# Performance work log

Measured on AMD Instinct MI355X. Metric: run time of the kernel, lower is better.

The kernel has to match this reference:

```python
import jax, jax.numpy as jnp
import numpy as np

N_HEADS = 8


def setup_inputs() -> dict:
    key = jax.random.key(0)
    qkv = jax.random.normal(key, (4, 1536, 2048), dtype=jnp.float32)
    return {"qkv": qkv}


def reference(qkv):
    bs, width, length = qkv.shape
    assert width % (3 * N_HEADS) == 0
    ch = width // (3 * N_HEADS)
    q, k, v = jnp.split(qkv, 3, axis=1)            # each [bs, H*C, T]
    scale = 1.0 / (ch ** 0.25)                      # 1/sqrt(sqrt(ch)) applied to both q and k
    q = (q * scale).reshape(bs * N_HEADS, ch, length)
    k = (k * scale).reshape(bs * N_HEADS, ch, length)
    v = v.reshape(bs * N_HEADS, ch, length)
    weight = jnp.einsum('bct,bcs->bts', q, k)       # [bs*H, T, T]
    weight = jax.nn.softmax(weight.astype(jnp.float32), axis=-1).astype(weight.dtype)
    a = jnp.einsum('bts,bcs->bct', weight, v)       # [bs*H, C, T]
    return a.reshape(bs, -1, length)
```

## Files before the change

kernel.cpp:

```cpp
#include <hip/hip_runtime.h>


typedef _Float16 half8  __attribute__((ext_vector_type(8)));
typedef _Float16 half4  __attribute__((ext_vector_type(4)));
typedef float    floatx4 __attribute__((ext_vector_type(4)));

constexpr int T    = 2048;
constexpr int TQ   = 128;
constexpr int TS   = 64;
constexpr int LDK  = 72;
constexpr int LDV  = 72;
constexpr int KHALF  = TS * LDK;
constexpr int SMEM_H = KHALF + 64 * LDV;
constexpr int NIT  = T / TS;
constexpr float QSCALE = 0.125f * 1.44269504088896340736f;

__device__ __forceinline__ half4 pack4(float a, float b, float c, float d) {
    half4 r;
    r[0] = (_Float16)a; r[1] = (_Float16)b;
    r[2] = (_Float16)c; r[3] = (_Float16)d;
    return r;
}

__global__ __launch_bounds__(512, 4)
void qkv_attn_kernel(const float* __restrict__ qkv, float* __restrict__ out) {
    __shared__ __align__(16) _Float16 smem[2][SMEM_H];

    const int tid  = threadIdx.x;
    const int wave = tid >> 6;
    const int lane = tid & 63;
    const int n16  = lane & 15;
    const int g    = lane >> 4;
    const int h    = wave >> 2;
    const int qg   = wave & 3;

    const int bx = blockIdx.x;
    const int hd = bx & 31;
    const int qt = bx >> 5;
    const int b  = hd >> 3;
    const int hh = hd & 7;
    const int q0 = qt * TQ;

    const float* __restrict__ qbase = qkv + (size_t)(b * 1536 + hh * 64) * T;
    const float* __restrict__ kbase = qkv + (size_t)(b * 1536 + 512 + hh * 64) * T;
    const float* __restrict__ vbase = qkv + (size_t)(b * 1536 + 1024 + hh * 64) * T;
    float* __restrict__ obase = out + (size_t)(b * 512 + hh * 64) * T;

    const bool kstage = (wave < 4);
    const int ptid = tid & 255;
    const int ks   = ((ptid >> 6) << 4) | (ptid & 15);
    const int kc4  = ((ptid >> 4) & 3) << 2;
    const int vc   = ptid >> 4;
    const int vt   = ptid & 15;
    const int vcol = 32 * (vt >> 3) + 8 * (vt & 3) + 4 * ((vt >> 2) & 1);

    float pre[16];
    auto prefetch = [&](int s0) {
        if (kstage) {
            const float* kg = kbase + s0 + ks;
#pragma unroll
            for (int i = 0; i < 4; ++i) {
                const int c = i * 16 + kc4;
#pragma unroll
                for (int j = 0; j < 4; ++j) pre[i * 4 + j] = kg[(c + j) * T];
            }
        } else {
            const float* vg = vbase + vc * T + s0 + vt * 4;
#pragma unroll
            for (int i = 0; i < 4; ++i) {
                const floatx4 vv = *(const floatx4*)&vg[i * 16 * T];
                pre[i * 4 + 0] = vv.x; pre[i * 4 + 1] = vv.y;
                pre[i * 4 + 2] = vv.z; pre[i * 4 + 3] = vv.w;
            }
        }
    };
    auto flush = [&](int buf) {
        if (kstage) {
            _Float16* kd = &smem[buf][ks * LDK];
#pragma unroll
            for (int i = 0; i < 4; ++i)
                *(half4*)&kd[i * 16 + kc4] =
                    pack4(pre[i * 4], pre[i * 4 + 1], pre[i * 4 + 2], pre[i * 4 + 3]);
        } else {
            _Float16* vd = &smem[buf][KHALF + vc * LDV + vcol];
#pragma unroll
            for (int i = 0; i < 4; ++i)
                *(half4*)&vd[i * 16 * LDV] =
                    pack4(pre[i * 4], pre[i * 4 + 1], pre[i * 4 + 2], pre[i * 4 + 3]);
        }
    };

    half8 bq[2][2];
    floatx4 oacc[4][2];
    float lsum[2];

#pragma unroll
    for (int qt2 = 0; qt2 < 2; ++qt2) {
        const int q = q0 + qg * 32 + qt2 * 16 + n16;
#pragma unroll
        for (int kcA = 0; kcA < 2; ++kcA)
#pragma unroll
            for (int j = 0; j < 8; ++j) {
                const int c = kcA * 32 + g * 8 + j;
                bq[qt2][kcA][j] = (_Float16)(qbase[c * T + q] * QSCALE);
            }
    }
#pragma unroll
    for (int mt = 0; mt < 4; ++mt)
#pragma unroll
        for (int qt2 = 0; qt2 < 2; ++qt2) oacc[mt][qt2] = (floatx4)(0.f);
    lsum[0] = 0.f; lsum[1] = 0.f;

    prefetch(0);
    flush(0);
    __syncthreads();

    for (int it = 0; it < NIT; ++it) {
        const int buf = it & 1;
        if (it + 1 < NIT) prefetch((it + 1) * TS);

        const _Float16* kb = &smem[buf][0];
        const _Float16* vb = &smem[buf][KHALF];

        floatx4 sacc[2][2];
#pragma unroll
        for (int sub = 0; sub < 2; ++sub) {
            const half8 ak0 = *(const half8*)&kb[((h * 2 + sub) * 16 + n16) * LDK + g * 8];
            const half8 ak1 = *(const half8*)&kb[((h * 2 + sub) * 16 + n16) * LDK + 32 + g * 8];
#pragma unroll
            for (int qt2 = 0; qt2 < 2; ++qt2) {
                floatx4 acc = (floatx4)(0.f);
                acc = __builtin_amdgcn_mfma_f32_16x16x32_f16(ak0, bq[qt2][0], acc, 0, 0, 0);
                acc = __builtin_amdgcn_mfma_f32_16x16x32_f16(ak1, bq[qt2][1], acc, 0, 0, 0);
                sacc[qt2][sub] = acc;
            }
        }
        half8 av[4];
#pragma unroll
        for (int mt = 0; mt < 4; ++mt)
            av[mt] = *(const half8*)&vb[(mt * 16 + n16) * LDV + h * 32 + g * 8];
#pragma unroll
        for (int qt2 = 0; qt2 < 2; ++qt2) {
            float pv[8];
#pragma unroll
            for (int sub = 0; sub < 2; ++sub)
#pragma unroll
                for (int r = 0; r < 4; ++r)
                    pv[sub * 4 + r] = __builtin_amdgcn_exp2f(sacc[qt2][sub][r]);
            lsum[qt2] += ((pv[0] + pv[1]) + (pv[2] + pv[3]))
                       + ((pv[4] + pv[5]) + (pv[6] + pv[7]));
            half8 bp;
#pragma unroll
            for (int i = 0; i < 8; ++i) bp[i] = (_Float16)pv[i];
#pragma unroll
            for (int mt = 0; mt < 4; ++mt)
                oacc[mt][qt2] = __builtin_amdgcn_mfma_f32_16x16x32_f16(
                    av[mt], bp, oacc[mt][qt2], 0, 0, 0);
        }

        if (it + 1 < NIT) flush(buf ^ 1);
        __syncthreads();
    }

    float* red = (float*)&smem[0][0];
    const int rbase = (qg * 64 + lane) * 36;
    if (h == 1) {
#pragma unroll
        for (int qt2 = 0; qt2 < 2; ++qt2)
#pragma unroll
            for (int mt = 0; mt < 4; ++mt)
                *(floatx4*)&red[rbase + (qt2 * 4 + mt) * 4] = oacc[mt][qt2];
        red[rbase + 32] = lsum[0];
        red[rbase + 33] = lsum[1];
    }
    __syncthreads();
    if (h == 0) {
#pragma unroll
        for (int qt2 = 0; qt2 < 2; ++qt2)
#pragma unroll
            for (int mt = 0; mt < 4; ++mt)
                oacc[mt][qt2] += *(const floatx4*)&red[rbase + (qt2 * 4 + mt) * 4];
        lsum[0] += red[rbase + 32];
        lsum[1] += red[rbase + 33];
#pragma unroll
        for (int qt2 = 0; qt2 < 2; ++qt2) {
            float l = lsum[qt2];
            l += __shfl_xor(l, 16);
            l += __shfl_xor(l, 32);
            const float linv = 1.0f / l;
            const int tcol = q0 + qg * 32 + qt2 * 16 + n16;
#pragma unroll
            for (int mt = 0; mt < 4; ++mt)
#pragma unroll
                for (int r = 0; r < 4; ++r)
                    obase[(mt * 16 + g * 4 + r) * T + tcol] = oacc[mt][qt2][r] * linv;
        }
    }
}

extern "C" void kernel_launch(void* const* d_in, const int* in_sizes, int n_in,
                              void* d_out, int out_size, void* d_ws, size_t ws_size,
                              hipStream_t stream) {
    const float* qkv = (const float*)d_in[0];
    float* out = (float*)d_out;
    qkv_attn_kernel<<<dim3(512), dim3(512), 0, stream>>>(qkv, out);
}
```

Measured before the change: 125.8 us.

## Halve query tile per block, double grid, and raise MFMA wave priority

The query tile per block drops from 128 to 64 rows, so each wave handles one 16-query sub-tile instead of two and the grid doubles to 1024 blocks. The launch-bounds occupancy hint rises from 4 to 8 blocks to match the lower register use. s_setprio is placed around the MFMA groups so matrix work is favoured over the loads of other waves. The trade-off is that each K/V tile is now fetched and converted to fp16 twice as often per query, which doubles global load and staging traffic for K and V.

```diff
diff --git a/kernel.cpp b/kernel.cpp
--- a/kernel.cpp
+++ b/kernel.cpp
@@ -6,7 +6,7 @@
 typedef float    floatx4 __attribute__((ext_vector_type(4)));
 
 constexpr int T    = 2048;
-constexpr int TQ   = 128;
+constexpr int TQ   = 64;
 constexpr int TS   = 64;
 constexpr int LDK  = 72;
 constexpr int LDV  = 72;
@@ -22,7 +22,7 @@
     return r;
 }
 
-__global__ __launch_bounds__(512, 4)
+__global__ __launch_bounds__(512, 8)
 void qkv_attn_kernel(const float* __restrict__ qkv, float* __restrict__ out) {
     __shared__ __align__(16) _Float16 smem[2][SMEM_H];
 
@@ -90,26 +90,22 @@
         }
     };
 
-    half8 bq[2][2];
-    floatx4 oacc[4][2];
-    float lsum[2];
+    half8 bq[2];
+    floatx4 oacc[4];
+    float lsum = 0.f;
 
-#pragma unroll
-    for (int qt2 = 0; qt2 < 2; ++qt2) {
-        const int q = q0 + qg * 32 + qt2 * 16 + n16;
+    {
+        const int q = q0 + qg * 16 + n16;
 #pragma unroll
         for (int kcA = 0; kcA < 2; ++kcA)
 #pragma unroll
             for (int j = 0; j < 8; ++j) {
                 const int c = kcA * 32 + g * 8 + j;
-                bq[qt2][kcA][j] = (_Float16)(qbase[c * T + q] * QSCALE);
+                bq[kcA][j] = (_Float16)(qbase[c * T + q] * QSCALE);
             }
     }
 #pragma unroll
-    for (int mt = 0; mt < 4; ++mt)
-#pragma unroll
-        for (int qt2 = 0; qt2 < 2; ++qt2) oacc[mt][qt2] = (floatx4)(0.f);
-    lsum[0] = 0.f; lsum[1] = 0.f;
+    for (int mt = 0; mt < 4; ++mt) oacc[mt] = (floatx4)(0.f);
 
     prefetch(0);
     flush(0);
@@ -122,40 +118,40 @@
         const _Float16* kb = &smem[buf][0];
         const _Float16* vb = &smem[buf][KHALF];
 
-        floatx4 sacc[2][2];
+        floatx4 sacc[2];
 #pragma unroll
         for (int sub = 0; sub < 2; ++sub) {
             const half8 ak0 = *(const half8*)&kb[((h * 2 + sub) * 16 + n16) * LDK + g * 8];
             const half8 ak1 = *(const half8*)&kb[((h * 2 + sub) * 16 + n16) * LDK + 32 + g * 8];
-#pragma unroll
-            for (int qt2 = 0; qt2 < 2; ++qt2) {
-                floatx4 acc = (floatx4)(0.f);
-                acc = __builtin_amdgcn_mfma_f32_16x16x32_f16(ak0, bq[qt2][0], acc, 0, 0, 0);
-                acc = __builtin_amdgcn_mfma_f32_16x16x32_f16(ak1, bq[qt2][1], acc, 0, 0, 0);
-                sacc[qt2][sub] = acc;
-            }
+            floatx4 acc = (floatx4)(0.f);
+            __builtin_amdgcn_s_setprio(1);
+            acc = __builtin_amdgcn_mfma_f32_16x16x32_f16(ak0, bq[0], acc, 0, 0, 0);
+            acc = __builtin_amdgcn_mfma_f32_16x16x32_f16(ak1, bq[1], acc, 0, 0, 0);
+            __builtin_amdgcn_s_setprio(0);
+            sacc[sub] = acc;
         }
         half8 av[4];
 #pragma unroll
         for (int mt = 0; mt < 4; ++mt)
             av[mt] = *(const half8*)&vb[(mt * 16 + n16) * LDV + h * 32 + g * 8];
-#pragma unroll
-        for (int qt2 = 0; qt2 < 2; ++qt2) {
+        {
             float pv[8];
 #pragma unroll
             for (int sub = 0; sub < 2; ++sub)
 #pragma unroll
                 for (int r = 0; r < 4; ++r)
-                    pv[sub * 4 + r] = __builtin_amdgcn_exp2f(sacc[qt2][sub][r]);
-            lsum[qt2] += ((pv[0] + pv[1]) + (pv[2] + pv[3]))
-                       + ((pv[4] + pv[5]) + (pv[6] + pv[7]));
+                    pv[sub * 4 + r] = __builtin_amdgcn_exp2f(sacc[sub][r]);
+            lsum += ((pv[0] + pv[1]) + (pv[2] + pv[3]))
+                  + ((pv[4] + pv[5]) + (pv[6] + pv[7]));
             half8 bp;
 #pragma unroll
             for (int i = 0; i < 8; ++i) bp[i] = (_Float16)pv[i];
+            __builtin_amdgcn_s_setprio(1);
 #pragma unroll
             for (int mt = 0; mt < 4; ++mt)
-                oacc[mt][qt2] = __builtin_amdgcn_mfma_f32_16x16x32_f16(
-                    av[mt], bp, oacc[mt][qt2], 0, 0, 0);
+                oacc[mt] = __builtin_amdgcn_mfma_f32_16x16x32_f16(
+                    av[mt], bp, oacc[mt], 0, 0, 0);
+            __builtin_amdgcn_s_setprio(0);
         }
 
         if (it + 1 < NIT) flush(buf ^ 1);
@@ -163,38 +159,29 @@
     }
 
     float* red = (float*)&smem[0][0];
-    const int rbase = (qg * 64 + lane) * 36;
+    const int rbase = (qg * 64 + lane) * 20;
     if (h == 1) {
 #pragma unroll
-        for (int qt2 = 0; qt2 < 2; ++qt2)
-#pragma unroll
-            for (int mt = 0; mt < 4; ++mt)
-                *(floatx4*)&red[rbase + (qt2 * 4 + mt) * 4] = oacc[mt][qt2];
-        red[rbase + 32] = lsum[0];
-        red[rbase + 33] = lsum[1];
+        for (int mt = 0; mt < 4; ++mt)
+            *(floatx4*)&red[rbase + mt * 4] = oacc[mt];
+        red[rbase + 16] = lsum;
     }
     __syncthreads();
     if (h == 0) {
 #pragma unroll
-        for (int qt2 = 0; qt2 < 2; ++qt2)
+        for (int mt = 0; mt < 4; ++mt)
+            oacc[mt] += *(const floatx4*)&red[rbase + mt * 4];
+        lsum += red[rbase + 16];
+        float l = lsum;
+        l += __shfl_xor(l, 16);
+        l += __shfl_xor(l, 32);
+        const float linv = 1.0f / l;
+        const int tcol = q0 + qg * 16 + n16;
 #pragma unroll
-            for (int mt = 0; mt < 4; ++mt)
-                oacc[mt][qt2] += *(const floatx4*)&red[rbase + (qt2 * 4 + mt) * 4];
-        lsum[0] += red[rbase + 32];
-        lsum[1] += red[rbase + 33];
+        for (int mt = 0; mt < 4; ++mt)
 #pragma unroll
-        for (int qt2 = 0; qt2 < 2; ++qt2) {
-            float l = lsum[qt2];
-            l += __shfl_xor(l, 16);
-            l += __shfl_xor(l, 32);
-            const float linv = 1.0f / l;
-            const int tcol = q0 + qg * 32 + qt2 * 16 + n16;
-#pragma unroll
-            for (int mt = 0; mt < 4; ++mt)
-#pragma unroll
-                for (int r = 0; r < 4; ++r)
-                    obase[(mt * 16 + g * 4 + r) * T + tcol] = oacc[mt][qt2][r] * linv;
-        }
+            for (int r = 0; r < 4; ++r)
+                obase[(mt * 16 + g * 4 + r) * T + tcol] = oacc[mt][r] * linv;
     }
 }
 
@@ -203,5 +190,5 @@
                               hipStream_t stream) {
     const float* qkv = (const float*)d_in[0];
     float* out = (float*)d_out;
-    qkv_attn_kernel<<<dim3(512), dim3(512), 0, stream>>>(qkv, out);
+    qkv_attn_kernel<<<dim3(1024), dim3(512), 0, stream>>>(qkv, out);
 }
```

Result: slower. 323.5 us (+157.2%).

## Split key span across two blocks with merge kernel; add MFMA priority hints

Applied to the files above, without the earlier changes.

Splits the 2048-key loop into two halves handled by separate blocks, doubling the grid from 512 to 1024 blocks. Each half writes unnormalised partial outputs and row sums to the output and a workspace, and a second merge kernel adds them and divides. This is meant to improve occupancy and wave count across the CUs, at the cost of an extra kernel launch and extra global read/write traffic for the partials. It also wraps the MFMA sections in s_setprio hints to favour matrix issue. Merging without a max shift is valid only because the kernel already skips max subtraction.

```diff
diff --git a/kernel.cpp b/kernel.cpp
--- a/kernel.cpp
+++ b/kernel.cpp
@@ -12,8 +12,12 @@
 constexpr int LDV  = 72;
 constexpr int KHALF  = TS * LDK;
 constexpr int SMEM_H = KHALF + 64 * LDV;
-constexpr int NIT  = T / TS;
 constexpr float QSCALE = 0.125f * 1.44269504088896340736f;
+
+constexpr int WS_L0 = 0;
+constexpr int WS_L1 = 65536;
+constexpr int WS_P1 = 131072;
+constexpr size_t WS_NEED_BYTES = (size_t)(WS_P1 + 4194304) * 4;
 
 __device__ __forceinline__ half4 pack4(float a, float b, float c, float d) {
     half4 r;
@@ -22,8 +26,13 @@
     return r;
 }
 
+template <int SSPAN_T>
 __global__ __launch_bounds__(512, 4)
-void qkv_attn_kernel(const float* __restrict__ qkv, float* __restrict__ out) {
+void qkv_attn_kernel(const float* __restrict__ qkv, float* __restrict__ out,
+                     float* __restrict__ ws) {
+    constexpr int  NIT   = SSPAN_T / TS;
+    constexpr bool SPLIT = (SSPAN_T != T);
+
     __shared__ __align__(16) _Float16 smem[2][SMEM_H];
 
     const int tid  = threadIdx.x;
@@ -34,12 +43,15 @@
     const int h    = wave >> 2;
     const int qg   = wave & 3;
 
-    const int bx = blockIdx.x;
-    const int hd = bx & 31;
-    const int qt = bx >> 5;
-    const int b  = hd >> 3;
-    const int hh = hd & 7;
-    const int q0 = qt * TQ;
+    const int bx  = blockIdx.x;
+    const int sh  = SPLIT ? (bx & 1) : 0;
+    const int pid = SPLIT ? (bx >> 1) : bx;
+    const int hd  = pid & 31;
+    const int qt  = pid >> 5;
+    const int b   = hd >> 3;
+    const int hh  = hd & 7;
+    const int q0  = qt * TQ;
+    const int sbase = sh * SSPAN_T;
 
     const float* __restrict__ qbase = qkv + (size_t)(b * 1536 + hh * 64) * T;
     const float* __restrict__ kbase = qkv + (size_t)(b * 1536 + 512 + hh * 64) * T;
@@ -111,13 +123,13 @@
         for (int qt2 = 0; qt2 < 2; ++qt2) oacc[mt][qt2] = (floatx4)(0.f);
     lsum[0] = 0.f; lsum[1] = 0.f;
 
-    prefetch(0);
+    prefetch(sbase);
     flush(0);
     __syncthreads();
 
     for (int it = 0; it < NIT; ++it) {
         const int buf = it & 1;
-        if (it + 1 < NIT) prefetch((it + 1) * TS);
+        if (it + 1 < NIT) prefetch(sbase + (it + 1) * TS);
 
         const _Float16* kb = &smem[buf][0];
         const _Float16* vb = &smem[buf][KHALF];
@@ -127,6 +139,7 @@
         for (int sub = 0; sub < 2; ++sub) {
             const half8 ak0 = *(const half8*)&kb[((h * 2 + sub) * 16 + n16) * LDK + g * 8];
             const half8 ak1 = *(const half8*)&kb[((h * 2 + sub) * 16 + n16) * LDK + 32 + g * 8];
+            __builtin_amdgcn_s_setprio(1);
 #pragma unroll
             for (int qt2 = 0; qt2 < 2; ++qt2) {
                 floatx4 acc = (floatx4)(0.f);
@@ -134,6 +147,7 @@
                 acc = __builtin_amdgcn_mfma_f32_16x16x32_f16(ak1, bq[qt2][1], acc, 0, 0, 0);
                 sacc[qt2][sub] = acc;
             }
+            __builtin_amdgcn_s_setprio(0);
         }
         half8 av[4];
 #pragma unroll
@@ -152,10 +166,12 @@
             half8 bp;
 #pragma unroll
             for (int i = 0; i < 8; ++i) bp[i] = (_Float16)pv[i];
+            __builtin_amdgcn_s_setprio(1);
 #pragma unroll
             for (int mt = 0; mt < 4; ++mt)
                 oacc[mt][qt2] = __builtin_amdgcn_mfma_f32_16x16x32_f16(
                     av[mt], bp, oacc[mt][qt2], 0, 0, 0);
+            __builtin_amdgcn_s_setprio(0);
         }
 
         if (it + 1 < NIT) flush(buf ^ 1);
@@ -182,20 +198,59 @@
                 oacc[mt][qt2] += *(const floatx4*)&red[rbase + (qt2 * 4 + mt) * 4];
         lsum[0] += red[rbase + 32];
         lsum[1] += red[rbase + 33];
-#pragma unroll
-        for (int qt2 = 0; qt2 < 2; ++qt2) {
-            float l = lsum[qt2];
-            l += __shfl_xor(l, 16);
-            l += __shfl_xor(l, 32);
-            const float linv = 1.0f / l;
-            const int tcol = q0 + qg * 32 + qt2 * 16 + n16;
-#pragma unroll
-            for (int mt = 0; mt < 4; ++mt)
-#pragma unroll
-                for (int r = 0; r < 4; ++r)
-                    obase[(mt * 16 + g * 4 + r) * T + tcol] = oacc[mt][qt2][r] * linv;
-        }
-    }
+
+        if constexpr (SPLIT) {
+            float* pdst = (sh == 0) ? obase
+                                    : ws + WS_P1 + (size_t)(b * 512 + hh * 64) * T;
+            float* ldst = ws + (sh == 0 ? WS_L0 : WS_L1) + (b * 8 + hh) * T;
+#pragma unroll
+            for (int qt2 = 0; qt2 < 2; ++qt2) {
+                float l = lsum[qt2];
+                l += __shfl_xor(l, 16);
+                l += __shfl_xor(l, 32);
+                const int tcol = q0 + qg * 32 + qt2 * 16 + n16;
+                if (g == 0) ldst[tcol] = l;
+#pragma unroll
+                for (int mt = 0; mt < 4; ++mt)
+#pragma unroll
+                    for (int r = 0; r < 4; ++r)
+                        pdst[(mt * 16 + g * 4 + r) * T + tcol] = oacc[mt][qt2][r];
+            }
+        } else {
+#pragma unroll
+            for (int qt2 = 0; qt2 < 2; ++qt2) {
+                float l = lsum[qt2];
+                l += __shfl_xor(l, 16);
+                l += __shfl_xor(l, 32);
+                const float linv = 1.0f / l;
+                const int tcol = q0 + qg * 32 + qt2 * 16 + n16;
+#pragma unroll
+                for (int mt = 0; mt < 4; ++mt)
+#pragma unroll
+                    for (int r = 0; r < 4; ++r)
+                        obase[(mt * 16 + g * 4 + r) * T + tcol] = oacc[mt][qt2][r] * linv;
+            }
+        }
+    }
+}
+
+__global__ __launch_bounds__(256)
+void qkv_merge_kernel(float* __restrict__ out, const float* __restrict__ ws) {
+    const int idx = blockIdx.x * 256 + threadIdx.x;
+    const size_t f = (size_t)idx * 4;
+    const int t   = (int)(f & (size_t)(T - 1));
+    const int row = (int)(f >> 11);
+    const int bh  = ((row >> 9) << 3) + ((row >> 6) & 7);
+    const floatx4 o  = *(const floatx4*)&out[f];
+    const floatx4 p  = *(const floatx4*)&ws[WS_P1 + f];
+    const floatx4 l0 = *(const floatx4*)&ws[WS_L0 + (size_t)bh * T + t];
+    const floatx4 l1 = *(const floatx4*)&ws[WS_L1 + (size_t)bh * T + t];
+    floatx4 r;
+    r.x = (o.x + p.x) / (l0.x + l1.x);
+    r.y = (o.y + p.y) / (l0.y + l1.y);
+    r.z = (o.z + p.z) / (l0.z + l1.z);
+    r.w = (o.w + p.w) / (l0.w + l1.w);
+    *(floatx4*)&out[f] = r;
 }
 
 extern "C" void kernel_launch(void* const* d_in, const int* in_sizes, int n_in,
@@ -203,5 +258,11 @@
                               hipStream_t stream) {
     const float* qkv = (const float*)d_in[0];
     float* out = (float*)d_out;
-    qkv_attn_kernel<<<dim3(512), dim3(512), 0, stream>>>(qkv, out);
-}
+    float* ws = (float*)d_ws;
+    if (ws != nullptr && ws_size >= WS_NEED_BYTES) {
+        qkv_attn_kernel<1024><<<dim3(1024), dim3(512), 0, stream>>>(qkv, out, ws);
+        qkv_merge_kernel<<<dim3(4096), dim3(256), 0, stream>>>(out, ws);
+    } else {
+        qkv_attn_kernel<2048><<<dim3(512), dim3(512), 0, stream>>>(qkv, out, ws);
+    }
+}
```

Measured after the change: 139.9 us. 1.11x slower.
